# Performance work log

Measured on AMD Instinct MI355X. Metric: run time of the kernel, lower is better.

## Reference

```python
import jax, jax.numpy as jnp
import numpy as np

B, D, H = 32768, 688, 4
DH = D // H          # 172 head dim (d_model // h, overrides ctor d_k)
MH = 128             # mlp hidden
EPS = 1e-5
SCALE = 1.0 / float(np.sqrt(DH))


def _ln(x, g, b):
    m = jnp.mean(x, -1, keepdims=True)
    v = jnp.var(x, -1, keepdims=True)  # biased var, matches torch LayerNorm
    return (x - m) / jnp.sqrt(v + EPS) * g + b


def setup_inputs() -> dict:
    key = jax.random.key(0)
    ks = jax.random.split(key, 16)
    w = lambda k, o, i: jax.random.normal(k, (o, i), jnp.float32) * 0.001  # init.normal_(std=0.001)
    z = lambda n: jnp.zeros((n,), jnp.float32)
    o = lambda n: jnp.ones((n,), jnp.float32)
    return dict(
        x=jax.random.normal(ks[0], (B, D), jnp.float32),
        x2=jax.random.normal(ks[1], (B, D), jnp.float32),
        Wq_v=w(ks[2], D, D), bq_v=z(D),
        Wk_v=w(ks[3], D, D), bk_v=z(D),
        Wv_v=w(ks[4], D, D), bv_v=z(D),
        Wq_i=w(ks[5], D, D), bq_i=z(D),
        Wk_i=w(ks[6], D, D), bk_i=z(D),
        Wv_i=w(ks[7], D, D), bv_i=z(D),
        Wo_v=w(ks[8], D, D), bo_v=z(D),
        Wo_i=w(ks[9], D, D), bo_i=z(D),
        ln1_g=o(D), ln1_b=z(D), ln2_g=o(D), ln2_b=z(D),
        ln3_g=o(D), ln3_b=z(D), ln4_g=o(D), ln4_b=z(D),
        m1v_W=w(ks[10], MH, D), m1v_b=z(MH),
        m2v_W=w(ks[11], D, MH), m2v_b=z(D),
        m1i_W=w(ks[12], MH, D), m1i_b=z(MH),
        m2i_W=w(ks[13], D, MH), m2i_b=z(D),
        coef=o(8),  # LearnableCoefficient 1..8, all init to 1.0
    )


def reference(x, x2,
              Wq_v, bq_v, Wk_v, bk_v, Wv_v, bv_v,
              Wq_i, bq_i, Wk_i, bk_i, Wv_i, bv_i,
              Wo_v, bo_v, Wo_i, bo_i,
              ln1_g, ln1_b, ln2_g, ln2_b, ln3_g, ln3_b, ln4_g, ln4_b,
              m1v_W, m1v_b, m2v_W, m2v_b, m1i_W, m1i_b, m2i_W, m2i_b,
              coef):
    rgb = _ln(x, ln1_g, ln1_b)
    ir = _ln(x2, ln2_g, ln2_b)
    proj = lambda t, W, b: (t @ W.T + b).reshape(-1, H, DH)  # (B, h, d_k)
    q_vis, k_vis, v_vis = proj(rgb, Wq_v, bq_v), proj(rgb, Wk_v, bk_v), proj(rgb, Wv_v, bv_v)
    q_ir, k_ir, v_ir = proj(ir, Wq_i, bq_i), proj(ir, Wk_i, bk_i), proj(ir, Wv_i, bv_i)
    # cross attention over heads: scores are (B, h, h)
    att_vis = jax.nn.softmax(jnp.einsum('bhd,bgd->bhg', q_ir, k_vis) * SCALE, -1)
    att_ir = jax.nn.softmax(jnp.einsum('bhd,bgd->bhg', q_vis, k_ir) * SCALE, -1)
    out_vis = jnp.einsum('bhg,bgd->bhd', att_vis, v_vis).reshape(-1, D) @ Wo_v.T + bo_v
    out_ir = jnp.einsum('bhg,bgd->bhd', att_ir, v_ir).reshape(-1, D) @ Wo_i.T + bo_i
    out_vis = coef[0] * x + coef[1] * out_vis
    out_ir = coef[2] * x2 + coef[3] * out_ir
    mv = jax.nn.gelu(_ln(out_vis, ln3_g, ln3_b) @ m1v_W.T + m1v_b, approximate=False) @ m2v_W.T + m2v_b
    mi = jax.nn.gelu(_ln(out_ir, ln4_g, ln4_b) @ m1i_W.T + m1i_b, approximate=False) @ m2i_W.T + m2i_b
    out_vis = coef[4] * out_vis + coef[5] * mv
    out_ir = coef[6] * out_ir + coef[7] * mi
    return out_vis, out_ir
```

## Files before the change

### kernel.cpp

```cpp
#include <hip/hip_runtime.h>
#include <cmath>


#define B_ROWS 32768
#define D_DIM  688
#define DP     768
#define DH_DIM 172
#define MH_DIM 128

typedef unsigned short ushort_t;
typedef __attribute__((ext_vector_type(8))) __bf16 bf16x8;
typedef __attribute__((ext_vector_type(4))) float  f32x4;

__device__ __forceinline__ float b2f(ushort_t u) {
    return __builtin_bit_cast(float, (unsigned int)u << 16);
}
__device__ __forceinline__ ushort_t f2bf(float f) {
    unsigned int u = __builtin_bit_cast(unsigned int, f);
    u += 0x7FFFu + ((u >> 16) & 1u);
    return (ushort_t)(u >> 16);
}

__device__ __forceinline__ void gl2lds16(const ushort_t* g, ushort_t* l) {
    __builtin_amdgcn_global_load_lds(
        (const __attribute__((address_space(1))) unsigned int*)g,
        (__attribute__((address_space(3))) unsigned int*)l, 16, 0, 0);
}

struct CvtJobs {
    const float* src[12];
    ushort_t*    dst[12];
    int O[12], Opad[12], Kin[12], Kpad[12];
    int bstart[13];
};

__global__ __launch_bounds__(256)
void cvt_all(CvtJobs jobs)
{
    int b = blockIdx.x;
    int j = 0;
    while (b >= jobs.bstart[j + 1]) ++j;
    const int t = (b - jobs.bstart[j]) * 256 + threadIdx.x;
    const int Kpad = jobs.Kpad[j];
    const int Kin  = jobs.Kin[j];
    const int cpr  = Kpad >> 3;
    if (t >= jobs.Opad[j] * cpr) return;
    const int o = t / cpr;
    const int c = t - o * cpr;
    unsigned int p0 = 0, p1 = 0, p2 = 0, p3 = 0;
    if (o < jobs.O[j] && (c * 8 + 8) <= Kin) {
        const float* s = jobs.src[j] + (size_t)o * Kin + c * 8;
        float4 f0 = reinterpret_cast<const float4*>(s)[0];
        float4 f1 = reinterpret_cast<const float4*>(s)[1];
        p0 = f2bf(f0.x) | ((unsigned int)f2bf(f0.y) << 16);
        p1 = f2bf(f0.z) | ((unsigned int)f2bf(f0.w) << 16);
        p2 = f2bf(f1.x) | ((unsigned int)f2bf(f1.y) << 16);
        p3 = f2bf(f1.z) | ((unsigned int)f2bf(f1.w) << 16);
    }
    *reinterpret_cast<uint4*>(jobs.dst[j] + (size_t)o * Kpad + c * 8) =
        make_uint4(p0, p1, p2, p3);
}

__global__ __launch_bounds__(256)
void pack_bias(const float* __restrict__ a0, const float* __restrict__ a1,
               const float* __restrict__ a2, const float* __restrict__ b0,
               const float* __restrict__ b1, const float* __restrict__ b2,
               float* __restrict__ dv, float* __restrict__ di)
{
    int t = blockIdx.x * 256 + threadIdx.x;
    if (t >= 2064) return;
    float v, w;
    if (t < 688)       { v = a0[t];        w = b0[t]; }
    else if (t < 1376) { v = a1[t - 688];  w = b1[t - 688]; }
    else               { v = a2[t - 1376]; w = b2[t - 1376]; }
    dv[t] = v; di[t] = w;
}

__global__ __launch_bounds__(256)
void ln_kernel(const float* __restrict__ Xv, const float* __restrict__ Xi,
               const float* __restrict__ gv, const float* __restrict__ bv,
               const float* __restrict__ gi, const float* __restrict__ bi,
               ushort_t* __restrict__ Yv, ushort_t* __restrict__ Yi)
{
    const int lane = threadIdx.x & 63;
    const int wave = threadIdx.x >> 6;
    const long w = (long)blockIdx.x * 4 + wave;
    const float* X; const float* g; const float* b; ushort_t* Y; long r;
    if (w < B_ROWS) { X = Xv; g = gv; b = bv; Y = Yv; r = w; }
    else            { X = Xi; g = gi; b = bi; Y = Yi; r = w - B_ROWS; }

    const float4* row = reinterpret_cast<const float4*>(X + r * D_DIM);
    float4 v0 = row[lane];
    float4 v1 = row[lane + 64];
    float4 v2 = make_float4(0.f, 0.f, 0.f, 0.f);
    if (lane < 44) v2 = row[lane + 128];

    float s  = v0.x + v0.y + v0.z + v0.w + v1.x + v1.y + v1.z + v1.w
             + v2.x + v2.y + v2.z + v2.w;
    float s2 = v0.x*v0.x + v0.y*v0.y + v0.z*v0.z + v0.w*v0.w
             + v1.x*v1.x + v1.y*v1.y + v1.z*v1.z + v1.w*v1.w
             + v2.x*v2.x + v2.y*v2.y + v2.z*v2.z + v2.w*v2.w;
#pragma unroll
    for (int m = 32; m; m >>= 1) { s += __shfl_xor(s, m); s2 += __shfl_xor(s2, m); }

    const float mean = s * (1.f / 688.f);
    const float var  = s2 * (1.f / 688.f) - mean * mean;
    const float rstd = rsqrtf(var + 1e-5f);

    const float4* g4 = reinterpret_cast<const float4*>(g);
    const float4* b4 = reinterpret_cast<const float4*>(b);
    ushort4* out4 = reinterpret_cast<ushort4*>(Y + r * DP);

    {
        float4 gg = g4[lane], bb = b4[lane];
        ushort4 o;
        o.x = f2bf((v0.x - mean) * rstd * gg.x + bb.x);
        o.y = f2bf((v0.y - mean) * rstd * gg.y + bb.y);
        o.z = f2bf((v0.z - mean) * rstd * gg.z + bb.z);
        o.w = f2bf((v0.w - mean) * rstd * gg.w + bb.w);
        out4[lane] = o;
    }
    {
        float4 gg = g4[lane + 64], bb = b4[lane + 64];
        ushort4 o;
        o.x = f2bf((v1.x - mean) * rstd * gg.x + bb.x);
        o.y = f2bf((v1.y - mean) * rstd * gg.y + bb.y);
        o.z = f2bf((v1.z - mean) * rstd * gg.z + bb.z);
        o.w = f2bf((v1.w - mean) * rstd * gg.w + bb.w);
        out4[lane + 64] = o;
    }
    if (lane < 44) {
        float4 gg = g4[lane + 128], bb = b4[lane + 128];
        ushort4 o;
        o.x = f2bf((v2.x - mean) * rstd * gg.x + bb.x);
        o.y = f2bf((v2.y - mean) * rstd * gg.y + bb.y);
        o.z = f2bf((v2.z - mean) * rstd * gg.z + bb.z);
        o.w = f2bf((v2.w - mean) * rstd * gg.w + bb.w);
        out4[lane + 128] = o;
    } else {
        out4[lane + 128] = make_ushort4(0, 0, 0, 0);
    }
}

__global__ __launch_bounds__(256)
void ln_bf16(const ushort_t* __restrict__ Xv, const ushort_t* __restrict__ Xi,
             const float* __restrict__ gv, const float* __restrict__ bv,
             const float* __restrict__ gi, const float* __restrict__ bi,
             ushort_t* __restrict__ Yv, ushort_t* __restrict__ Yi)
{
    const int lane = threadIdx.x & 63;
    const int wave = threadIdx.x >> 6;
    const long w = (long)blockIdx.x * 4 + wave;
    const ushort_t* X; const float* g; const float* b; ushort_t* Y; long r;
    if (w < B_ROWS) { X = Xv; g = gv; b = bv; Y = Yv; r = w; }
    else            { X = Xi; g = gi; b = bi; Y = Yi; r = w - B_ROWS; }

    const ushort4* row = reinterpret_cast<const ushort4*>(X + r * D_DIM);
    ushort4 u0 = row[lane];
    ushort4 u1 = row[lane + 64];
    ushort4 u2 = make_ushort4(0, 0, 0, 0);
    if (lane < 44) u2 = row[lane + 128];

    float f0x = b2f(u0.x), f0y = b2f(u0.y), f0z = b2f(u0.z), f0w = b2f(u0.w);
    float f1x = b2f(u1.x), f1y = b2f(u1.y), f1z = b2f(u1.z), f1w = b2f(u1.w);
    float f2x = b2f(u2.x), f2y = b2f(u2.y), f2z = b2f(u2.z), f2w = b2f(u2.w);

    float s  = f0x + f0y + f0z + f0w + f1x + f1y + f1z + f1w + f2x + f2y + f2z + f2w;
    float s2 = f0x*f0x + f0y*f0y + f0z*f0z + f0w*f0w
             + f1x*f1x + f1y*f1y + f1z*f1z + f1w*f1w
             + f2x*f2x + f2y*f2y + f2z*f2z + f2w*f2w;
#pragma unroll
    for (int m = 32; m; m >>= 1) { s += __shfl_xor(s, m); s2 += __shfl_xor(s2, m); }

    const float mean = s * (1.f / 688.f);
    const float var  = s2 * (1.f / 688.f) - mean * mean;
    const float rstd = rsqrtf(var + 1e-5f);

    const float4* g4 = reinterpret_cast<const float4*>(g);
    const float4* b4 = reinterpret_cast<const float4*>(b);
    ushort4* out4 = reinterpret_cast<ushort4*>(Y + r * DP);

    {
        float4 gg = g4[lane], bb = b4[lane];
        ushort4 o;
        o.x = f2bf((f0x - mean) * rstd * gg.x + bb.x);
        o.y = f2bf((f0y - mean) * rstd * gg.y + bb.y);
        o.z = f2bf((f0z - mean) * rstd * gg.z + bb.z);
        o.w = f2bf((f0w - mean) * rstd * gg.w + bb.w);
        out4[lane] = o;
    }
    {
        float4 gg = g4[lane + 64], bb = b4[lane + 64];
        ushort4 o;
        o.x = f2bf((f1x - mean) * rstd * gg.x + bb.x);
        o.y = f2bf((f1y - mean) * rstd * gg.y + bb.y);
        o.z = f2bf((f1z - mean) * rstd * gg.z + bb.z);
        o.w = f2bf((f1w - mean) * rstd * gg.w + bb.w);
        out4[lane + 64] = o;
    }
    if (lane < 44) {
        float4 gg = g4[lane + 128], bb = b4[lane + 128];
        ushort4 o;
        o.x = f2bf((f2x - mean) * rstd * gg.x + bb.x);
        o.y = f2bf((f2y - mean) * rstd * gg.y + bb.y);
        o.z = f2bf((f2z - mean) * rstd * gg.z + bb.z);
        o.w = f2bf((f2w - mean) * rstd * gg.w + bb.w);
        out4[lane + 128] = o;
    } else {
        out4[lane + 128] = make_ushort4(0, 0, 0, 0);
    }
}

template<int MODE>
__global__ __launch_bounds__(512, 1)
void gemm8(const ushort_t* __restrict__ A0, const ushort_t* __restrict__ A1,
           const ushort_t* __restrict__ W0, const ushort_t* __restrict__ W1,
           const float* __restrict__ bias0, const float* __restrict__ bias1,
           ushort_t* __restrict__ out0, ushort_t* __restrict__ out1,
           const float* __restrict__ res0, const float* __restrict__ res1,
           const float* __restrict__ coef, int ca0, int cb0, int ca1, int cb1,
           int NBn, int N, int K, int lda, int ldw, int ldo)
{
    __shared__ __align__(16) ushort_t lds8[65536];

    const int q8 = gridDim.x >> 3;
    const int v  = (blockIdx.x & 7) * q8 + (blockIdx.x >> 3);
    const int nb = v % NBn;
    const int tmp = v / NBn;
    const int mb = tmp & 127;
    const int zz = tmp >> 7;

    const ushort_t* A = zz ? A1 : A0;
    const ushort_t* W = zz ? W1 : W0;
    const float* bias = zz ? bias1 : bias0;
    ushort_t* outp    = zz ? out1 : out0;
    const float* resid = zz ? res1 : res0;
    const int ca = zz ? ca1 : ca0;
    const int cb = zz ? cb1 : cb0;

    const int tid  = threadIdx.x;
    const int lane = tid & 63;
    const int wave = tid >> 6;
    const int wrow = wave >> 2;
    const int wcol = wave & 3;
    const int m0 = mb * 256;
    const int n0 = nb * 256;
    const int rl16 = lane & 15;
    const int q4   = lane >> 4;

    const int r0 = tid >> 3;
    const int u0 = tid & 7;
    const int swz0 = ((u0 ^ (r0 & 7)) * 8);

    f32x4 acc[8][4];
#pragma unroll
    for (int i = 0; i < 8; ++i)
#pragma unroll
        for (int j = 0; j < 4; ++j)
            acc[i][j] = f32x4{0.f, 0.f, 0.f, 0.f};

    const int NT = K >> 6;

#define STAGE8(mat, rbase, ld, kt, hf, tilebase) do {                              \
    const ushort_t* _s = (mat) + (size_t)((rbase) + (hf)*128 + r0) * (ld)          \
                         + (kt)*64 + swz0;                                         \
    gl2lds16(_s,                 (tilebase) + (hf)*8192 + wave*512);               \
    gl2lds16(_s + 64*(size_t)(ld), (tilebase) + (hf)*8192 + 4096 + wave*512);      \
} while (0)

#define RD_A(base, mib, kkv) do {                                                  \
    _Pragma("unroll")                                                              \
    for (int i = 0; i < 4; ++i) {                                                  \
        const int row_ = wrow*128 + ((mib)+i)*16 + rl16;                           \
        const int un_  = (((kkv) >> 3) + q4) ^ (lane & 7);                         \
        af[i] = *reinterpret_cast<const bf16x8*>((base) + row_*64 + un_*8);        \
    } } while (0)

#define RD_B(base, kkv) do {                                                       \
    _Pragma("unroll")                                                              \
    for (int j = 0; j < 4; ++j) {                                                  \
        const int row_ = wcol*64 + j*16 + rl16;                                    \
        const int un_  = (((kkv) >> 3) + q4) ^ (lane & 7);                         \
        bw[j] = *reinterpret_cast<const bf16x8*>((base) + row_*64 + un_*8);        \
    } } while (0)

#define MFMA16(mib) do {                                                           \
    __builtin_amdgcn_s_setprio(1);                                                 \
    _Pragma("unroll")                                                              \
    for (int i = 0; i < 4; ++i)                                                    \
    _Pragma("unroll")                                                              \
    for (int j = 0; j < 4; ++j)                                                    \
        acc[(mib)+i][j] =                                                          \
            __builtin_amdgcn_mfma_f32_16x16x32_bf16(af[i], bw[j], acc[(mib)+i][j], \
                                                    0, 0, 0);                      \
    __builtin_amdgcn_s_setprio(0);                                                 \
} while (0)

    STAGE8(A, m0, lda, 0, 0, lds8);
    STAGE8(A, m0, lda, 0, 1, lds8);
    STAGE8(W, n0, ldw, 0, 0, lds8 + 32768);
    STAGE8(W, n0, ldw, 0, 1, lds8 + 32768);
    STAGE8(W, n0, ldw, 1, 0, lds8 + 49152);
    asm volatile("s_waitcnt vmcnt(2)" ::: "memory");
    __builtin_amdgcn_s_barrier();

    for (int t = 0; t < NT; ++t) {
        ushort_t* const Ab  = lds8 + ((t & 1) * 16384);
        ushort_t* const Bb  = lds8 + 32768 + ((t & 1) * 16384);
        ushort_t* const An  = lds8 + (((t + 1) & 1) * 16384);
        ushort_t* const Bn1 = lds8 + 32768 + (((t + 1) & 1) * 16384);
        ushort_t* const Bn2 = Bb;
        const int tn1 = (t + 1 < NT) ? t + 1 : NT - 1;
        const int tn2 = (t + 2 < NT) ? t + 2 : NT - 1;

        bf16x8 af[4], bw[4];

        RD_A(Ab, 0, 0);
        RD_B(Bb, 0);
        STAGE8(A, m0, lda, tn1, 0, An);
        STAGE8(W, n0, ldw, tn1, 1, Bn1);
        __builtin_amdgcn_s_barrier();
        MFMA16(0);
        __builtin_amdgcn_s_barrier();

        RD_A(Ab, 4, 0);
        STAGE8(A, m0, lda, tn1, 1, An);
        __builtin_amdgcn_s_barrier();
        MFMA16(4);
        __builtin_amdgcn_s_barrier();

        RD_A(Ab, 0, 32);
        RD_B(Bb, 32);
        __builtin_amdgcn_s_barrier();
        MFMA16(0);
        __builtin_amdgcn_s_barrier();

        RD_A(Ab, 4, 32);
        STAGE8(W, n0, ldw, tn2, 0, Bn2);
        asm volatile("s_waitcnt vmcnt(2)" ::: "memory");
        __builtin_amdgcn_s_barrier();
        MFMA16(4);
        __builtin_amdgcn_s_barrier();
    }

    asm volatile("s_waitcnt vmcnt(0)" ::: "memory");
    __builtin_amdgcn_s_barrier();

    ushort_t* const Cl = lds8;
#pragma unroll
    for (int mi = 0; mi < 8; ++mi)
#pragma unroll
        for (int nj = 0; nj < 4; ++nj)
#pragma unroll
            for (int r = 0; r < 4; ++r) {
                const int row  = wrow*128 + mi*16 + q4*4 + r;
                const int colL = wcol*64 + nj*16 + rl16;
                const int blk  = (colL >> 3) ^ (((row >> 2) & 3) << 1);
                Cl[row*256 + blk*8 + (colL & 7)] = f2bf(acc[mi][nj][r]);
            }
    __syncthreads();

    float cA = 0.f, cB = 1.f;
    if constexpr (MODE == 1) { cA = coef[ca]; cB = coef[cb]; }
#pragma unroll
    for (int it2 = 0; it2 < 16; ++it2) {
        const int c   = it2 * 512 + tid;
        const int row = c >> 5;
        const int lb  = c & 31;
        const int gcol = n0 + lb * 8;
        if (gcol >= N) continue;
        const int pb = lb ^ (((row >> 2) & 3) << 1);
        uint4 pv = *reinterpret_cast<const uint4*>(Cl + row*256 + pb*8);
        const ushort_t* pu = (const ushort_t*)&pv;
        float4 b0 = *reinterpret_cast<const float4*>(bias + gcol);
        float4 b1 = *reinterpret_cast<const float4*>(bias + gcol + 4);
        const float bb[8] = {b0.x, b0.y, b0.z, b0.w, b1.x, b1.y, b1.z, b1.w};
        const size_t idx = (size_t)(m0 + row) * ldo + gcol;
        ushort_t o[8];
        if constexpr (MODE == 0) {
#pragma unroll
            for (int k = 0; k < 8; ++k) o[k] = f2bf(b2f(pu[k]) + bb[k]);
        } else {
            const float* rp = resid + idx;
            float4 r0_ = reinterpret_cast<const float4*>(rp)[0];
            float4 r1_ = reinterpret_cast<const float4*>(rp)[1];
            const float rr[8] = {r0_.x, r0_.y, r0_.z, r0_.w, r1_.x, r1_.y, r1_.z, r1_.w};
#pragma unroll
            for (int k = 0; k < 8; ++k)
                o[k] = f2bf(cA * rr[k] + cB * (b2f(pu[k]) + bb[k]));
        }
        *reinterpret_cast<uint4*>(outp + idx) = *reinterpret_cast<uint4*>(o);
    }
#undef STAGE8
#undef RD_A
#undef RD_B
#undef MFMA16
}

template<int MODE>
__global__ __launch_bounds__(256, 4)
void gemm2(const ushort_t* __restrict__ A0, const ushort_t* __restrict__ A1,
           const ushort_t* __restrict__ W0, const ushort_t* __restrict__ W1,
           const float* __restrict__ bias0, const float* __restrict__ bias1,
           void* __restrict__ out0, void* __restrict__ out1,
           const void* __restrict__ res0, const void* __restrict__ res1,
           const float* __restrict__ coef,
           int ca0, int cb0, int ca1, int cb1,
           int NBn, int N, int K, int lda, int ldw, int ldo)
{
    __shared__ __align__(16) ushort_t smem[16384];
    ushort_t* As = smem;
    ushort_t* Bs = smem + 8192;

    const int q  = gridDim.x >> 3;
    const int vb = (blockIdx.x & 7) * q + (blockIdx.x >> 3);
    const int nb = vb % NBn;
    const int tmp = vb / NBn;
    const int mb = tmp & 255;
    const int zz = tmp >> 8;

    const ushort_t* A = zz ? A1 : A0;
    const ushort_t* W = zz ? W1 : W0;
    const float* bias = zz ? bias1 : bias0;
    void* outp        = zz ? out1 : out0;
    const void* resid = zz ? res1 : res0;
    const int ca = zz ? ca1 : ca0;
    const int cb = zz ? cb1 : cb0;

    const int tid  = threadIdx.x;
    const int lane = tid & 63;
    const int wave = tid >> 6;
    const int m0 = mb * 128;
    const int n0 = nb * 128;
    const int wm = (wave >> 1) * 64;
    const int wn = (wave & 1) * 64;

    const int s0 = wave * 128 + lane;
    const int s1 = s0 + 64;
    const ushort_t* pa0 = A + (size_t)(m0 + (s0 >> 2)) * lda + (s0 & 3) * 8;
    const ushort_t* pa1 = A + (size_t)(m0 + (s1 >> 2)) * lda + (s1 & 3) * 8;
    const ushort_t* pb0 = W + (size_t)(n0 + (s0 >> 2)) * ldw + (s0 & 3) * 8;
    const ushort_t* pb1 = W + (size_t)(n0 + (s1 >> 2)) * ldw + (s1 & 3) * 8;

    f32x4 acc[4][4];
#pragma unroll
    for (int i = 0; i < 4; ++i)
#pragma unroll
        for (int j = 0; j < 4; ++j)
            acc[i][j] = f32x4{0.f, 0.f, 0.f, 0.f};

    const int ko = (lane >> 4) * 8;
    const int rl = lane & 15;
    const int nkt = K / 32;

    auto stage = [&](int buf, int kt) {
        const int kof = kt * 32;
        ushort_t* ad = As + buf * 4096 + wave * 1024;
        ushort_t* bd = Bs + buf * 4096 + wave * 1024;
        gl2lds16(pa0 + kof, ad);
        gl2lds16(pa1 + kof, ad + 512);
        gl2lds16(pb0 + kof, bd);
        gl2lds16(pb1 + kof, bd + 512);
    };

    stage(0, 0);
    __syncthreads();

    for (int kt = 0; kt < nkt; ++kt) {
        const int cur = kt & 1;
        if (kt + 1 < nkt) stage(cur ^ 1, kt + 1);

        const ushort_t* Ab = As + cur * 4096;
        const ushort_t* Bb = Bs + cur * 4096;
        bf16x8 af[4], bwv[4];
#pragma unroll
        for (int i = 0; i < 4; ++i) {
            af[i]  = *reinterpret_cast<const bf16x8*>(&Ab[(wm + i * 16 + rl) * 32 + ko]);
            bwv[i] = *reinterpret_cast<const bf16x8*>(&Bb[(wn + i * 16 + rl) * 32 + ko]);
        }
#pragma unroll
        for (int i = 0; i < 4; ++i)
#pragma unroll
            for (int j = 0; j < 4; ++j)
                acc[i][j] = __builtin_amdgcn_mfma_f32_16x16x32_bf16(af[i], bwv[j], acc[i][j], 0, 0, 0);
        __syncthreads();
    }

    float cA = 0.f, cB = 1.f;
    if constexpr (MODE == 3) { cA = coef[ca]; cB = coef[cb]; }
    const int rb = (lane >> 4) * 4;
    const int cl = lane & 15;
    ushort_t* C = smem;
#pragma unroll
    for (int j = 0; j < 4; ++j) {
        const int lcol = wn + j * 16 + cl;
        const int col = n0 + lcol;
        const float bc = (col < N) ? bias[col] : 0.f;
#pragma unroll
        for (int i = 0; i < 4; ++i) {
            const int lrow = wm + i * 16 + rb;
#pragma unroll
            for (int r = 0; r < 4; ++r) {
                float val = acc[i][j][r] + bc;
                if constexpr (MODE == 2)
                    val = 0.5f * val * (1.0f + erff(val * 0.70710678118654752f));
                C[(lrow + r) * 128 + lcol] = f2bf(val);
            }
        }
    }
    __syncthreads();

#pragma unroll
    for (int p = 0; p < 8; ++p) {
        const int c = tid + p * 256;
        const int lrow = c >> 4;
        const int lcl = (c & 15) * 8;
        const int gcol = n0 + lcl;
        if (gcol >= N) continue;
        const size_t idx = (size_t)(m0 + lrow) * ldo + gcol;
        uint4 pv = *reinterpret_cast<const uint4*>(&C[lrow * 128 + lcl]);
        if constexpr (MODE == 2) {
            *reinterpret_cast<uint4*>((ushort_t*)outp + idx) = pv;
        } else {
            uint4 rv = *reinterpret_cast<const uint4*>((const ushort_t*)resid + idx);
            const ushort_t* pu = (const ushort_t*)&pv;
            const ushort_t* ru = (const ushort_t*)&rv;
            float o[8];
#pragma unroll
            for (int k = 0; k < 8; ++k)
                o[k] = cA * b2f(ru[k]) + cB * b2f(pu[k]);
            float4* op = reinterpret_cast<float4*>((float*)outp + idx);
            op[0] = make_float4(o[0], o[1], o[2], o[3]);
            op[1] = make_float4(o[4], o[5], o[6], o[7]);
        }
    }
}

__global__ __launch_bounds__(256)
void attn_kernel(const ushort_t* __restrict__ qkv_v, const ushort_t* __restrict__ qkv_i,
                 ushort_t* __restrict__ ctx_v, ushort_t* __restrict__ ctx_i)
{
    const int lane = threadIdx.x & 63;
    const int wave = threadIdx.x >> 6;
    const long r = (long)blockIdx.x * 4 + wave;
    const ushort_t* bv = qkv_v + r * 2064;
    const ushort_t* bi = qkv_i + r * 2064;

    float sv[4][4], si[4][4];
#pragma unroll
    for (int h = 0; h < 4; ++h)
#pragma unroll
        for (int g = 0; g < 4; ++g) { sv[h][g] = 0.f; si[h][g] = 0.f; }

    float vvr[3][4], vir[3][4];
#pragma unroll
    for (int it = 0; it < 3; ++it) {
        const int d = lane + it * 64;
        const bool ok = d < DH_DIM;
        float qv[4], kv[4], qi[4], ki[4];
#pragma unroll
        for (int h = 0; h < 4; ++h) {
            const int o = h * DH_DIM + d;
            qv[h]      = ok ? b2f(bv[o]) : 0.f;
            kv[h]      = ok ? b2f(bv[D_DIM + o]) : 0.f;
            vvr[it][h] = ok ? b2f(bv[2 * D_DIM + o]) : 0.f;
            qi[h]      = ok ? b2f(bi[o]) : 0.f;
            ki[h]      = ok ? b2f(bi[D_DIM + o]) : 0.f;
            vir[it][h] = ok ? b2f(bi[2 * D_DIM + o]) : 0.f;
        }
#pragma unroll
        for (int h = 0; h < 4; ++h)
#pragma unroll
            for (int g = 0; g < 4; ++g) {
                sv[h][g] += qi[h] * kv[g];
                si[h][g] += qv[h] * ki[g];
            }
    }

#pragma unroll
    for (int h = 0; h < 4; ++h)
#pragma unroll
        for (int g = 0; g < 4; ++g) {
            float a = sv[h][g], b = si[h][g];
#pragma unroll
            for (int m = 32; m; m >>= 1) { a += __shfl_xor(a, m); b += __shfl_xor(b, m); }
            sv[h][g] = a; si[h][g] = b;
        }

    const float scale = 0.07624928516630235f;
    float av[4][4], ai[4][4];
#pragma unroll
    for (int h = 0; h < 4; ++h) {
        float m1 = fmaxf(fmaxf(sv[h][0], sv[h][1]), fmaxf(sv[h][2], sv[h][3])) * scale;
        float m2 = fmaxf(fmaxf(si[h][0], si[h][1]), fmaxf(si[h][2], si[h][3])) * scale;
        float d1 = 0.f, d2 = 0.f;
#pragma unroll
        for (int g = 0; g < 4; ++g) {
            av[h][g] = expf(sv[h][g] * scale - m1); d1 += av[h][g];
            ai[h][g] = expf(si[h][g] * scale - m2); d2 += ai[h][g];
        }
        const float r1 = 1.f / d1, r2 = 1.f / d2;
#pragma unroll
        for (int g = 0; g < 4; ++g) { av[h][g] *= r1; ai[h][g] *= r2; }
    }

#pragma unroll
    for (int it = 0; it < 3; ++it) {
        const int d = lane + it * 64;
        if (d < DH_DIM) {
#pragma unroll
            for (int h = 0; h < 4; ++h) {
                float cv = av[h][0] * vvr[it][0] + av[h][1] * vvr[it][1]
                         + av[h][2] * vvr[it][2] + av[h][3] * vvr[it][3];
                float ci = ai[h][0] * vir[it][0] + ai[h][1] * vir[it][1]
                         + ai[h][2] * vir[it][2] + ai[h][3] * vir[it][3];
                ctx_v[r * DP + h * DH_DIM + d] = f2bf(cv);
                ctx_i[r * DP + h * DH_DIM + d] = f2bf(ci);
            }
        }
    }
    for (int z = lane; z < 80; z += 64) {
        ctx_v[r * DP + 688 + z] = 0;
        ctx_i[r * DP + 688 + z] = 0;
    }
}

extern "C" void kernel_launch(void* const* d_in, const int* in_sizes, int n_in,
                              void* d_out, int out_size, void* d_ws, size_t ws_size,
                              hipStream_t stream)
{
    if (n_in < 35) return;
    const float* x     = (const float*)d_in[0];
    const float* x2    = (const float*)d_in[1];
    const float* Wq_v  = (const float*)d_in[2];
    const float* bq_v  = (const float*)d_in[3];
    const float* Wk_v  = (const float*)d_in[4];
    const float* bk_v  = (const float*)d_in[5];
    const float* Wv_v  = (const float*)d_in[6];
    const float* bv_v  = (const float*)d_in[7];
    const float* Wq_i  = (const float*)d_in[8];
    const float* bq_i  = (const float*)d_in[9];
    const float* Wk_i  = (const float*)d_in[10];
    const float* bk_i  = (const float*)d_in[11];
    const float* Wv_i  = (const float*)d_in[12];
    const float* bv_i  = (const float*)d_in[13];
    const float* Wo_v  = (const float*)d_in[14];
    const float* bo_v  = (const float*)d_in[15];
    const float* Wo_i  = (const float*)d_in[16];
    const float* bo_i  = (const float*)d_in[17];
    const float* ln1_g = (const float*)d_in[18];
    const float* ln1_b = (const float*)d_in[19];
    const float* ln2_g = (const float*)d_in[20];
    const float* ln2_b = (const float*)d_in[21];
    const float* ln3_g = (const float*)d_in[22];
    const float* ln3_b = (const float*)d_in[23];
    const float* ln4_g = (const float*)d_in[24];
    const float* ln4_b = (const float*)d_in[25];
    const float* m1v_W = (const float*)d_in[26];
    const float* m1v_b = (const float*)d_in[27];
    const float* m2v_W = (const float*)d_in[28];
    const float* m2v_b = (const float*)d_in[29];
    const float* m1i_W = (const float*)d_in[30];
    const float* m1i_b = (const float*)d_in[31];
    const float* m2i_W = (const float*)d_in[32];
    const float* m2i_b = (const float*)d_in[33];
    const float* coef  = (const float*)d_in[34];

    const size_t BDP = (size_t)B_ROWS * DP;
    const size_t BD  = (size_t)B_ROWS * D_DIM;

    char* ws = (char*)d_ws;
    size_t off = 0;
    auto give = [&](size_t bytes) {
        char* p = ws + off;
        off += (bytes + 255) & ~(size_t)255;
        return p;
    };
    ushort_t* Wcat_v = (ushort_t*)give(2304ull * DP * 2);
    ushort_t* Wcat_i = (ushort_t*)give(2304ull * DP * 2);
    ushort_t* Wo_vb  = (ushort_t*)give(768ull * DP * 2);
    ushort_t* Wo_ib  = (ushort_t*)give(768ull * DP * 2);
    ushort_t* m1vb   = (ushort_t*)give(128ull * DP * 2);
    ushort_t* m1ib   = (ushort_t*)give(128ull * DP * 2);
    ushort_t* m2vb   = (ushort_t*)give(768ull * 128 * 2);
    ushort_t* m2ib   = (ushort_t*)give(768ull * 128 * 2);
    float*    bcat_v = (float*)give(2064 * 4);
    float*    bcat_i = (float*)give(2064 * 4);
    char* regX = give(BDP * 2 * 2);
    char* regQ = give((size_t)B_ROWS * 2064 * 2 * 2);
    char* regG = give((size_t)B_ROWS * MH_DIM * 2 * 2);
    if (ws_size < off) return;

    ushort_t* xn_v  = (ushort_t*)regX;
    ushort_t* xn_i  = xn_v + BDP;
    ushort_t* ctx_v = xn_v;
    ushort_t* ctx_i = xn_i;
    ushort_t* h_v   = ctx_v;
    ushort_t* h_i   = ctx_i;
    ushort_t* qkv_v = (ushort_t*)regQ;
    ushort_t* qkv_i = qkv_v + (size_t)B_ROWS * 2064;
    ushort_t* ovb   = (ushort_t*)regQ;
    ushort_t* oib   = ovb + BD;
    ushort_t* g_v   = (ushort_t*)regG;
    ushort_t* g_i   = g_v + (size_t)B_ROWS * MH_DIM;

    float* ov = (float*)d_out;
    float* oi = ov + BD;

    CvtJobs J;
    const float* srcs[12] = {Wq_v, Wk_v, Wv_v, Wq_i, Wk_i, Wv_i,
                             Wo_v, Wo_i, m1v_W, m1i_W, m2v_W, m2i_W};
    ushort_t* dsts[12] = {Wcat_v, Wcat_v + 688 * DP, Wcat_v + 1376 * DP,
                          Wcat_i, Wcat_i + 688 * DP, Wcat_i + 1376 * DP,
                          Wo_vb, Wo_ib, m1vb, m1ib, m2vb, m2ib};
    int Os[12]    = {688, 688, 688, 688, 688, 688, 688, 688, 128, 128, 688, 688};
    int Opads[12] = {688, 688, 928, 688, 688, 928, 768, 768, 128, 128, 768, 768};
    int Kins[12]  = {688, 688, 688, 688, 688, 688, 688, 688, 688, 688, 128, 128};
    int Kpads[12] = {DP, DP, DP, DP, DP, DP, DP, DP, DP, DP, 128, 128};
    int bs = 0;
    for (int j = 0; j < 12; ++j) {
        J.src[j] = srcs[j]; J.dst[j] = dsts[j];
        J.O[j] = Os[j]; J.Opad[j] = Opads[j]; J.Kin[j] = Kins[j]; J.Kpad[j] = Kpads[j];
        J.bstart[j] = bs;
        bs += (Opads[j] * (Kpads[j] >> 3) + 255) / 256;
    }
    J.bstart[12] = bs;
    cvt_all<<<dim3(bs), dim3(256), 0, stream>>>(J);

    pack_bias<<<dim3(9), dim3(256), 0, stream>>>(bq_v, bk_v, bv_v, bq_i, bk_i, bv_i,
                                                 bcat_v, bcat_i);

    ln_kernel<<<dim3(2 * B_ROWS / 4), dim3(256), 0, stream>>>(
        x, x2, ln1_g, ln1_b, ln2_g, ln2_b, xn_v, xn_i);

    gemm8<0><<<dim3(128 * 9 * 2), dim3(512), 0, stream>>>(
        xn_v, xn_i, Wcat_v, Wcat_i, bcat_v, bcat_i, qkv_v, qkv_i,
        nullptr, nullptr, nullptr, 0, 0, 0, 0, 9, 2064, DP, DP, DP, 2064);

    attn_kernel<<<dim3(B_ROWS / 4), dim3(256), 0, stream>>>(qkv_v, qkv_i, ctx_v, ctx_i);

    gemm8<1><<<dim3(128 * 3 * 2), dim3(512), 0, stream>>>(
        ctx_v, ctx_i, Wo_vb, Wo_ib, bo_v, bo_i, ovb, oib,
        x, x2, coef, 0, 1, 2, 3, 3, 688, DP, DP, DP, 688);

    ln_bf16<<<dim3(2 * B_ROWS / 4), dim3(256), 0, stream>>>(
        ovb, oib, ln3_g, ln3_b, ln4_g, ln4_b, h_v, h_i);

    gemm2<2><<<dim3(256 * 1 * 2), dim3(256), 0, stream>>>(
        h_v, h_i, m1vb, m1ib, m1v_b, m1i_b, g_v, g_i,
        nullptr, nullptr, nullptr, 0, 0, 0, 0, 1, 128, DP, DP, DP, 128);

    gemm2<3><<<dim3(256 * 6 * 2), dim3(256), 0, stream>>>(
        g_v, g_i, m2vb, m2ib, m2v_b, m2i_b, ov, oi,
        ovb, oib, coef, 4, 5, 6, 7, 6, 688, 128, 128, 128, 688);
}
```

Baseline: 702.0 us.

## Fuse LN3/LN4 with first MLP GEMM and shrink K padding to 704

```diff
diff --git a/kernel.cpp b/kernel.cpp
--- a/kernel.cpp
+++ b/kernel.cpp
@@ -4,7 +4,7 @@
 
 #define B_ROWS 32768
 #define D_DIM  688
-#define DP     768
+#define DP     704
 #define DH_DIM 172
 #define MH_DIM 128
 
@@ -137,76 +137,7 @@
         o.z = f2bf((v2.z - mean) * rstd * gg.z + bb.z);
         o.w = f2bf((v2.w - mean) * rstd * gg.w + bb.w);
         out4[lane + 128] = o;
-    } else {
-        out4[lane + 128] = make_ushort4(0, 0, 0, 0);
-    }
-}
-
-__global__ __launch_bounds__(256)
-void ln_bf16(const ushort_t* __restrict__ Xv, const ushort_t* __restrict__ Xi,
-             const float* __restrict__ gv, const float* __restrict__ bv,
-             const float* __restrict__ gi, const float* __restrict__ bi,
-             ushort_t* __restrict__ Yv, ushort_t* __restrict__ Yi)
-{
-    const int lane = threadIdx.x & 63;
-    const int wave = threadIdx.x >> 6;
-    const long w = (long)blockIdx.x * 4 + wave;
-    const ushort_t* X; const float* g; const float* b; ushort_t* Y; long r;
-    if (w < B_ROWS) { X = Xv; g = gv; b = bv; Y = Yv; r = w; }
-    else            { X = Xi; g = gi; b = bi; Y = Yi; r = w - B_ROWS; }
-
-    const ushort4* row = reinterpret_cast<const ushort4*>(X + r * D_DIM);
-    ushort4 u0 = row[lane];
-    ushort4 u1 = row[lane + 64];
-    ushort4 u2 = make_ushort4(0, 0, 0, 0);
-    if (lane < 44) u2 = row[lane + 128];
-
-    float f0x = b2f(u0.x), f0y = b2f(u0.y), f0z = b2f(u0.z), f0w = b2f(u0.w);
-    float f1x = b2f(u1.x), f1y = b2f(u1.y), f1z = b2f(u1.z), f1w = b2f(u1.w);
-    float f2x = b2f(u2.x), f2y = b2f(u2.y), f2z = b2f(u2.z), f2w = b2f(u2.w);
-
-    float s  = f0x + f0y + f0z + f0w + f1x + f1y + f1z + f1w + f2x + f2y + f2z + f2w;
-    float s2 = f0x*f0x + f0y*f0y + f0z*f0z + f0w*f0w
-             + f1x*f1x + f1y*f1y + f1z*f1z + f1w*f1w
-             + f2x*f2x + f2y*f2y + f2z*f2z + f2w*f2w;
-#pragma unroll
-    for (int m = 32; m; m >>= 1) { s += __shfl_xor(s, m); s2 += __shfl_xor(s2, m); }
-
-    const float mean = s * (1.f / 688.f);
-    const float var  = s2 * (1.f / 688.f) - mean * mean;
-    const float rstd = rsqrtf(var + 1e-5f);
-
-    const float4* g4 = reinterpret_cast<const float4*>(g);
-    const float4* b4 = reinterpret_cast<const float4*>(b);
-    ushort4* out4 = reinterpret_cast<ushort4*>(Y + r * DP);
-
-    {
-        float4 gg = g4[lane], bb = b4[lane];
-        ushort4 o;
-        o.x = f2bf((f0x - mean) * rstd * gg.x + bb.x);
-        o.y = f2bf((f0y - mean) * rstd * gg.y + bb.y);
-        o.z = f2bf((f0z - mean) * rstd * gg.z + bb.z);
-        o.w = f2bf((f0w - mean) * rstd * gg.w + bb.w);
-        out4[lane] = o;
-    }
-    {
-        float4 gg = g4[lane + 64], bb = b4[lane + 64];
-        ushort4 o;
-        o.x = f2bf((f1x - mean) * rstd * gg.x + bb.x);
-        o.y = f2bf((f1y - mean) * rstd * gg.y + bb.y);
-        o.z = f2bf((f1z - mean) * rstd * gg.z + bb.z);
-        o.w = f2bf((f1w - mean) * rstd * gg.w + bb.w);
-        out4[lane + 64] = o;
-    }
-    if (lane < 44) {
-        float4 gg = g4[lane + 128], bb = b4[lane + 128];
-        ushort4 o;
-        o.x = f2bf((f2x - mean) * rstd * gg.x + bb.x);
-        o.y = f2bf((f2y - mean) * rstd * gg.y + bb.y);
-        o.z = f2bf((f2z - mean) * rstd * gg.z + bb.z);
-        o.w = f2bf((f2w - mean) * rstd * gg.w + bb.w);
-        out4[lane + 128] = o;
-    } else {
+    } else if (lane < 48) {
         out4[lane + 128] = make_ushort4(0, 0, 0, 0);
     }
 }
@@ -502,8 +433,6 @@
 #pragma unroll
             for (int r = 0; r < 4; ++r) {
                 float val = acc[i][j][r] + bc;
-                if constexpr (MODE == 2)
-                    val = 0.5f * val * (1.0f + erff(val * 0.70710678118654752f));
                 C[(lrow + r) * 128 + lcol] = f2bf(val);
             }
         }
@@ -519,20 +448,150 @@
         if (gcol >= N) continue;
         const size_t idx = (size_t)(m0 + lrow) * ldo + gcol;
         uint4 pv = *reinterpret_cast<const uint4*>(&C[lrow * 128 + lcl]);
-        if constexpr (MODE == 2) {
-            *reinterpret_cast<uint4*>((ushort_t*)outp + idx) = pv;
-        } else {
-            uint4 rv = *reinterpret_cast<const uint4*>((const ushort_t*)resid + idx);
-            const ushort_t* pu = (const ushort_t*)&pv;
-            const ushort_t* ru = (const ushort_t*)&rv;
-            float o[8];
+        uint4 rv = *reinterpret_cast<const uint4*>((const ushort_t*)resid + idx);
+        const ushort_t* pu = (const ushort_t*)&pv;
+        const ushort_t* ru = (const ushort_t*)&rv;
+        float o[8];
+#pragma unroll
+        for (int k = 0; k < 8; ++k)
+            o[k] = cA * b2f(ru[k]) + cB * b2f(pu[k]);
+        float4* op = reinterpret_cast<float4*>((float*)outp + idx);
+        op[0] = make_float4(o[0], o[1], o[2], o[3]);
+        op[1] = make_float4(o[4], o[5], o[6], o[7]);
+    }
+}
+
+__global__ __launch_bounds__(256)
+void lnmlp1(const ushort_t* __restrict__ ov0, const ushort_t* __restrict__ ov1,
+            const float* __restrict__ g0, const float* __restrict__ b0,
+            const float* __restrict__ g1, const float* __restrict__ b1,
+            const ushort_t* __restrict__ W10, const ushort_t* __restrict__ W11,
+            const float* __restrict__ mb0, const float* __restrict__ mb1,
+            ushort_t* __restrict__ out0, ushort_t* __restrict__ out1)
+{
+    __shared__ __align__(16) ushort_t hraw[64 * 712];
+    __shared__ float glds[704];
+    __shared__ float blds[704];
+    __shared__ float mlds[64];
+    __shared__ float rlds[64];
+
+    const int zz = blockIdx.y;
+    const ushort_t* ovb = zz ? ov1 : ov0;
+    const float* lg = zz ? g1 : g0;
+    const float* lb = zz ? b1 : b0;
+    const ushort_t* W1 = zz ? W11 : W10;
+    const float* mbias = zz ? mb1 : mb0;
+    ushort_t* outp = zz ? out1 : out0;
+
+    const int tid  = threadIdx.x;
+    const int lane = tid & 63;
+    const int wv   = tid >> 6;
+    const long r0  = (long)blockIdx.x * 64;
+
+    if (tid < 176) {
+        float4 gg = make_float4(0, 0, 0, 0), bb = make_float4(0, 0, 0, 0);
+        if (tid < 172) {
+            gg = reinterpret_cast<const float4*>(lg)[tid];
+            bb = reinterpret_cast<const float4*>(lb)[tid];
+        }
+        reinterpret_cast<float4*>(glds)[tid] = gg;
+        reinterpret_cast<float4*>(blds)[tid] = bb;
+    }
+
+#pragma unroll
+    for (int it = 0; it < 22; ++it) {
+        const int c = it * 256 + tid;
+        const int row = c / 88;
+        const int u = c - row * 88;
+        uint4 vv = make_uint4(0, 0, 0, 0);
+        if (u < 86)
+            vv = *reinterpret_cast<const uint4*>(ovb + (r0 + row) * 688 + u * 8);
+        *reinterpret_cast<uint4*>(&hraw[row * 712 + u * 8]) = vv;
+    }
+    __syncthreads();
+
+    for (int rr = 0; rr < 16; ++rr) {
+        const int row = wv * 16 + rr;
+        const ushort_t* hp = &hraw[row * 712];
+        ushort4 a0 = *reinterpret_cast<const ushort4*>(hp + lane * 4);
+        ushort4 a1 = *reinterpret_cast<const ushort4*>(hp + 256 + lane * 4);
+        ushort4 a2 = make_ushort4(0, 0, 0, 0);
+        if (lane < 44) a2 = *reinterpret_cast<const ushort4*>(hp + 512 + lane * 4);
+        float e[12] = {b2f(a0.x), b2f(a0.y), b2f(a0.z), b2f(a0.w),
+                       b2f(a1.x), b2f(a1.y), b2f(a1.z), b2f(a1.w),
+                       b2f(a2.x), b2f(a2.y), b2f(a2.z), b2f(a2.w)};
+        float s = 0.f, s2 = 0.f;
+#pragma unroll
+        for (int k = 0; k < 12; ++k) { s += e[k]; s2 += e[k] * e[k]; }
+#pragma unroll
+        for (int m = 32; m; m >>= 1) { s += __shfl_xor(s, m); s2 += __shfl_xor(s2, m); }
+        if (lane == 0) {
+            const float mean = s * (1.f / 688.f);
+            const float var  = s2 * (1.f / 688.f) - mean * mean;
+            mlds[row] = mean;
+            rlds[row] = rsqrtf(var + 1e-5f);
+        }
+    }
+    __syncthreads();
+
+#pragma unroll
+    for (int it = 0; it < 22; ++it) {
+        const int c = it * 256 + tid;
+        if (c < 5504) {
+            const int row = c / 86;
+            const int u = c - row * 86;
+            uint4 vv = *reinterpret_cast<const uint4*>(&hraw[row * 712 + u * 8]);
+            const float mean = mlds[row], rstd = rlds[row];
+            const ushort_t* pe = (const ushort_t*)&vv;
+            ushort_t o[8];
 #pragma unroll
             for (int k = 0; k < 8; ++k)
-                o[k] = cA * b2f(ru[k]) + cB * b2f(pu[k]);
-            float4* op = reinterpret_cast<float4*>((float*)outp + idx);
-            op[0] = make_float4(o[0], o[1], o[2], o[3]);
-            op[1] = make_float4(o[4], o[5], o[6], o[7]);
-        }
+                o[k] = f2bf((b2f(pe[k]) - mean) * rstd * glds[u * 8 + k] + blds[u * 8 + k]);
+            *reinterpret_cast<uint4*>(&hraw[row * 712 + u * 8]) = *reinterpret_cast<uint4*>(o);
+        }
+    }
+    __syncthreads();
+
+    const int rl16 = lane & 15;
+    const int q4   = lane >> 4;
+    f32x4 acc[4][2];
+#pragma unroll
+    for (int i = 0; i < 4; ++i) { acc[i][0] = f32x4{0,0,0,0}; acc[i][1] = f32x4{0,0,0,0}; }
+
+    for (int kt = 0; kt < 11; ++kt) {
+#pragma unroll
+        for (int kk = 0; kk < 64; kk += 32) {
+            bf16x8 af[4], bw[2];
+#pragma unroll
+            for (int n = 0; n < 2; ++n)
+                bw[n] = *reinterpret_cast<const bf16x8*>(
+                    W1 + (size_t)(wv * 32 + n * 16 + rl16) * 704 + kt * 64 + kk + q4 * 8);
+#pragma unroll
+            for (int i = 0; i < 4; ++i)
+                af[i] = *reinterpret_cast<const bf16x8*>(
+                    &hraw[(i * 16 + rl16) * 712 + kt * 64 + kk + q4 * 8]);
+#pragma unroll
+            for (int i = 0; i < 4; ++i)
+#pragma unroll
+                for (int n = 0; n < 2; ++n)
+                    acc[i][n] = __builtin_amdgcn_mfma_f32_16x16x32_bf16(
+                        af[i], bw[n], acc[i][n], 0, 0, 0);
+        }
+    }
+
+    const int rb = q4 * 4;
+#pragma unroll
+    for (int n = 0; n < 2; ++n) {
+        const int col = wv * 32 + n * 16 + rl16;
+        const float bc = mbias[col];
+#pragma unroll
+        for (int i = 0; i < 4; ++i)
+#pragma unroll
+            for (int r = 0; r < 4; ++r) {
+                float val = acc[i][n][r] + bc;
+                val = 0.5f * val * (1.0f + erff(val * 0.70710678118654752f));
+                outp[(r0 + i * 16 + rb + r) * 128 + col] = f2bf(val);
+            }
     }
 }
 
@@ -619,9 +678,9 @@
             }
         }
     }
-    for (int z = lane; z < 80; z += 64) {
-        ctx_v[r * DP + 688 + z] = 0;
-        ctx_i[r * DP + 688 + z] = 0;
+    if (lane < 16) {
+        ctx_v[r * DP + 688 + lane] = 0;
+        ctx_i[r * DP + 688 + lane] = 0;
     }
 }
 
@@ -695,8 +754,6 @@
     ushort_t* xn_i  = xn_v + BDP;
     ushort_t* ctx_v = xn_v;
     ushort_t* ctx_i = xn_i;
-    ushort_t* h_v   = ctx_v;
-    ushort_t* h_i   = ctx_i;
     ushort_t* qkv_v = (ushort_t*)regQ;
     ushort_t* qkv_i = qkv_v + (size_t)B_ROWS * 2064;
     ushort_t* ovb   = (ushort_t*)regQ;
@@ -743,12 +800,8 @@
         ctx_v, ctx_i, Wo_vb, Wo_ib, bo_v, bo_i, ovb, oib,
         x, x2, coef, 0, 1, 2, 3, 3, 688, DP, DP, DP, 688);
 
-    ln_bf16<<<dim3(2 * B_ROWS / 4), dim3(256), 0, stream>>>(
-        ovb, oib, ln3_g, ln3_b, ln4_g, ln4_b, h_v, h_i);
-
-    gemm2<2><<<dim3(256 * 1 * 2), dim3(256), 0, stream>>>(
-        h_v, h_i, m1vb, m1ib, m1v_b, m1i_b, g_v, g_i,
-        nullptr, nullptr, nullptr, 0, 0, 0, 0, 1, 128, DP, DP, DP, 128);
+    lnmlp1<<<dim3(B_ROWS / 64, 2), dim3(256), 0, stream>>>(
+        ovb, oib, ln3_g, ln3_b, ln4_g, ln4_b, m1vb, m1ib, m1v_b, m1i_b, g_v, g_i);
 
     gemm2<3><<<dim3(256 * 6 * 2), dim3(256), 0, stream>>>(
         g_v, g_i, m2vb, m2ib, m2v_b, m2i_b, ov, oi,
```

Measured after the change: 707.7 us. About the same (+0.8%).
